# Optimization experiments

Measured on AMD Instinct MI355X. Metric: run time of the kernel, lower is better.

The kernel has to match this reference:

```python
import jax, jax.numpy as jnp
import numpy as np

D_MODEL = 1024
N_HEADS = 16
D_K = D_MODEL // N_HEADS
BATCH = 4
SEQ = 2048


def setup_inputs() -> dict:
    key = jax.random.key(0)
    ks = jax.random.split(key, 12)
    s = 1.0 / np.sqrt(D_MODEL)
    inp = {
        "query": jax.random.normal(ks[0], (BATCH, SEQ, D_MODEL), jnp.float32),
        "key": jax.random.normal(ks[1], (BATCH, SEQ, D_MODEL), jnp.float32),
        "value": jax.random.normal(ks[2], (BATCH, SEQ, D_MODEL), jnp.float32),
        # causal mask: True = masked (ignored), broadcastable over batch/heads
        "mask": jnp.triu(jnp.ones((SEQ, SEQ), bool), k=1)[None, None, :, :],
        "w_q": jax.random.normal(ks[3], (D_MODEL, D_MODEL), jnp.float32) * s,
        "b_q": jax.random.normal(ks[4], (D_MODEL,), jnp.float32) * s,
        "w_k": jax.random.normal(ks[5], (D_MODEL, D_MODEL), jnp.float32) * s,
        "b_k": jax.random.normal(ks[6], (D_MODEL,), jnp.float32) * s,
        "w_v": jax.random.normal(ks[7], (D_MODEL, D_MODEL), jnp.float32) * s,
        "b_v": jax.random.normal(ks[8], (D_MODEL,), jnp.float32) * s,
        "w_o": jax.random.normal(ks[9], (D_MODEL, D_MODEL), jnp.float32) * s,
        "b_o": jax.random.normal(ks[10], (D_MODEL,), jnp.float32) * s,
    }
    return inp


def _split_heads(x):
    # (B, S, D) -> (B, H, S, d_k)
    b, s, _ = x.shape
    return x.reshape(b, s, N_HEADS, D_K).transpose(0, 2, 1, 3)


def reference(query, key, value, mask, w_q, b_q, w_k, b_k, w_v, b_v, w_o, b_o):
    # torch Linear: y = x @ W.T + b
    q = _split_heads(query @ w_q.T + b_q)
    k = _split_heads(key @ w_k.T + b_k)
    v = _split_heads(value @ w_v.T + b_v)
    scale = 1.0 / jnp.sqrt(jnp.asarray(D_K, q.dtype))
    scores = jnp.einsum("bhqd,bhkd->bhqk", q, k) * scale
    scores = jnp.where(mask, jnp.asarray(-jnp.inf, scores.dtype), scores)
    weights = jax.nn.softmax(scores, axis=-1)  # dropout p=0.0 (eval)
    attn = jnp.einsum("bhqk,bhkd->bhqd", weights, v)
    b = attn.shape[0]
    attn = attn.transpose(0, 2, 1, 3).reshape(b, -1, D_MODEL)
    return attn @ w_o.T + b_o
```

## Files before the change

### kernel.cpp

```cpp
#include <hip/hip_runtime.h>

#define S_LEN 2048
#define DMODEL 1024
#define H_CNT 16
#define DK 64
#define BATCH 4

typedef __attribute__((ext_vector_type(8))) short short8;
typedef __attribute__((ext_vector_type(4))) float f32x4;
typedef __attribute__((ext_vector_type(16))) float f32x16;

static __device__ __forceinline__ short f2bf(float f) {
  union { float f; unsigned u; } x; x.f = f;
  unsigned r = x.u + 0x7fffu + ((x.u >> 16) & 1u);
  return (short)(r >> 16);
}

static __device__ __forceinline__ unsigned cvt_pk_bf16(float lo, float hi) {
  unsigned r;
  asm("v_cvt_pk_bf16_f32 %0, %1, %2" : "=v"(r) : "v"(lo), "v"(hi));
  return r;
}

static __device__ __forceinline__ void gl_lds16(const short* g, short* l) {
  __builtin_amdgcn_global_load_lds((const __attribute__((address_space(1))) void*)g,
                                   (__attribute__((address_space(3))) void*)l, 16, 0, 0);
}

__global__ __launch_bounds__(256) void cast_kernel(const float* __restrict__ src,
                                                   short* __restrict__ dst, int n8) {
  int i = blockIdx.x * 256 + threadIdx.x;
  if (i >= n8) return;
  const float4* s4 = (const float4*)src;
  float4 a = s4[2 * i], b = s4[2 * i + 1];
  short8 o;
  o[0] = f2bf(a.x); o[1] = f2bf(a.y); o[2] = f2bf(a.z); o[3] = f2bf(a.w);
  o[4] = f2bf(b.x); o[5] = f2bf(b.y); o[6] = f2bf(b.z); o[7] = f2bf(b.w);
  ((short8*)dst)[i] = o;
}

template <int MODE>
__global__ __launch_bounds__(256) void gemm_bt(const short* __restrict__ A,
                                               const short* __restrict__ B,
                                               const float* __restrict__ bias,
                                               void* __restrict__ Cout,
                                               int M, int N, int K, float scl) {
  __shared__ short Sab[(128 + 64) * 32];
  const int tid = threadIdx.x;
  const int lane = tid & 63, wid = tid >> 6;
  const int lin = blockIdx.x;
  const int w = (lin & 7) * 128 + (lin >> 3);
  int bx, by;
  if (MODE == 1) { bx = w >> 3; by = w & 7; }
  else           { bx = w & 15; by = w >> 4; }
  const int m0 = by * 128, n0 = bx * 64;
  const int wr = wid * 32;
  const int lrow = lane & 15, lk8 = (lane >> 4) * 8;

  const int l4 = lane >> 2, lc = (lane & 3) * 8;
  const short* gsrc[3];
  short* ldst[3];
#pragma unroll
  for (int i = 0; i < 3; i++) {
    int c = wid * 3 + i;
    ldst[i] = &Sab[c * 512];
    if (c < 8) gsrc[i] = &A[(size_t)(m0 + c * 16 + l4) * K + lc];
    else       gsrc[i] = &B[(size_t)(n0 + (c - 8) * 16 + l4) * K + lc];
  }

  f32x4 acc[2][4] = {};

  for (int k0 = 0; k0 < K; k0 += 32) {
#pragma unroll
    for (int i = 0; i < 3; i++) gl_lds16(gsrc[i] + k0, ldst[i]);
    __syncthreads();
    short8 af[2], bfr[4];
#pragma unroll
    for (int m = 0; m < 2; m++) af[m] = *(const short8*)(&Sab[(wr + m * 16 + lrow) * 32 + lk8]);
#pragma unroll
    for (int n = 0; n < 4; n++) bfr[n] = *(const short8*)(&Sab[(128 + n * 16 + lrow) * 32 + lk8]);
#pragma unroll
    for (int m = 0; m < 2; m++)
#pragma unroll
      for (int n = 0; n < 4; n++)
        acc[m][n] = __builtin_amdgcn_mfma_f32_16x16x32_bf16(af[m], bfr[n], acc[m][n], 0, 0, 0);
    __syncthreads();
  }

  const int g4 = (lane >> 4) * 4;
#pragma unroll
  for (int n = 0; n < 4; n++) {
    const int col = n0 + n * 16 + lrow;
#pragma unroll
    for (int m = 0; m < 2; m++) {
#pragma unroll
      for (int i = 0; i < 4; i++) {
        const int row = m0 + wr + m * 16 + g4 + i;
        float val = acc[m][n][i];
        if (MODE == 0) {
          val = (val + bias[col]) * scl;
          int b = row >> 11, s2 = row & 2047, h = col >> 6, d = col & 63;
          ((short*)Cout)[((size_t)(b * H_CNT + h) * S_LEN + s2) * DK + d] = f2bf(val);
        } else if (MODE == 1) {
          val = val + bias[row];
          int h = row >> 6, d = row & 63, b = col >> 11, s2 = col & 2047;
          ((short*)Cout)[((size_t)(b * H_CNT + h) * DK + d) * S_LEN + s2] = f2bf(val);
        } else {
          val = val + bias[col];
          ((float*)Cout)[(size_t)row * N + col] = val;
        }
      }
    }
  }
}

__global__ __launch_bounds__(256, 4) void attn2_kernel(const short* __restrict__ Q,
                                                       const short* __restrict__ Kc,
                                                       const short* __restrict__ Vt,
                                                       short* __restrict__ Oout) {
  const int bh = blockIdx.y;
  const int j = blockIdx.x;
  const int wid = threadIdx.x >> 6, lane = threadIdx.x & 63;
  const int qt = (wid == 0) ? j : (wid == 1) ? (31 - j) : (wid == 2) ? (32 + j) : (63 - j);
  const int q0 = qt * 32;
  const int ql = lane & 31, hl = lane >> 5;

  const short* Qb = Q + (size_t)bh * S_LEN * DK;
  const short* Kb = Kc + (size_t)bh * S_LEN * DK;
  const short* Vb = Vt + (size_t)bh * DK * S_LEN;

  short8 qf[4];
#pragma unroll
  for (int kk = 0; kk < 4; kk++)
    qf[kk] = *(const short8*)(&Qb[(q0 + ql) * DK + kk * 16 + hl * 8]);

  f32x16 oacc[2] = {};
  float mr = -1e30f, lr = 0.f;

  const int ntiles = qt + 1;
  for (int t = 0; t < ntiles; t++) {
    const int kv0 = t * 32;
    f32x16 st = {};
#pragma unroll
    for (int kk = 0; kk < 4; kk++) {
      short8 kf = *(const short8*)(&Kb[(kv0 + ql) * DK + kk * 16 + hl * 8]);
      st = __builtin_amdgcn_mfma_f32_32x32x16_bf16(kf, qf[kk], st, 0, 0, 0);
    }
    short8 vf[2][2];
#pragma unroll
    for (int td = 0; td < 2; td++)
#pragma unroll
      for (int kk = 0; kk < 2; kk++)
        vf[td][kk] = *(const short8*)(&Vb[(size_t)(td * 32 + ql) * S_LEN + kv0 + kk * 16 + hl * 8]);

    float p[16];
#pragma unroll
    for (int r = 0; r < 16; r++) p[r] = st[r];
    if (t == ntiles - 1) {
#pragma unroll
      for (int r = 0; r < 16; r++) {
        int kvr = (r & 3) + 8 * (r >> 2) + 4 * hl;
        if (kvr > ql) p[r] = -1e30f;
      }
    }
    float pm = p[0];
#pragma unroll
    for (int r = 1; r < 16; r++) pm = fmaxf(pm, p[r]);
    pm = fmaxf(pm, __shfl_xor(pm, 32, 64));
    if (!__all(pm <= mr + 8.f)) {
      float mnew = fmaxf(mr, pm);
      float al = __builtin_amdgcn_exp2f(mr - mnew);
      lr *= al;
#pragma unroll
      for (int td = 0; td < 2; td++)
#pragma unroll
        for (int r = 0; r < 16; r++) oacc[td][r] *= al;
      mr = mnew;
    }
    float rs = 0.f;
#pragma unroll
    for (int r = 0; r < 16; r++) {
      p[r] = __builtin_amdgcn_exp2f(p[r] - mr);
      rs += p[r];
    }
    rs += __shfl_xor(rs, 32, 64);
    lr += rs;

    unsigned wpk[8];
#pragma unroll
    for (int tt = 0; tt < 8; tt++) wpk[tt] = cvt_pk_bf16(p[2 * tt], p[2 * tt + 1]);
    union { short8 s; unsigned u[4]; } bf0, bf1;
    {
      unsigned xa = __shfl_xor((int)wpk[2], 32, 64), xb = __shfl_xor((int)wpk[0], 32, 64);
      bf0.u[0] = hl ? xa : wpk[0];
      bf0.u[2] = hl ? wpk[2] : xb;
    }
    {
      unsigned xa = __shfl_xor((int)wpk[3], 32, 64), xb = __shfl_xor((int)wpk[1], 32, 64);
      bf0.u[1] = hl ? xa : wpk[1];
      bf0.u[3] = hl ? wpk[3] : xb;
    }
    {
      unsigned xa = __shfl_xor((int)wpk[6], 32, 64), xb = __shfl_xor((int)wpk[4], 32, 64);
      bf1.u[0] = hl ? xa : wpk[4];
      bf1.u[2] = hl ? wpk[6] : xb;
    }
    {
      unsigned xa = __shfl_xor((int)wpk[7], 32, 64), xb = __shfl_xor((int)wpk[5], 32, 64);
      bf1.u[1] = hl ? xa : wpk[5];
      bf1.u[3] = hl ? wpk[7] : xb;
    }

#pragma unroll
    for (int td = 0; td < 2; td++) {
      oacc[td] = __builtin_amdgcn_mfma_f32_32x32x16_bf16(vf[td][0], bf0.s, oacc[td], 0, 0, 0);
      oacc[td] = __builtin_amdgcn_mfma_f32_32x32x16_bf16(vf[td][1], bf1.s, oacc[td], 0, 0, 0);
    }
  }

  const float inv = __builtin_amdgcn_rcpf(lr);
  const int b = bh >> 4, h = bh & 15;
  unsigned* ob = (unsigned*)Oout + ((size_t)b * S_LEN + q0 + ql) * (DMODEL / 2) + h * (DK / 2);
#pragma unroll
  for (int td = 0; td < 2; td++)
#pragma unroll
    for (int tt = 0; tt < 8; tt++) {
      unsigned pkv = cvt_pk_bf16(oacc[td][2 * tt] * inv, oacc[td][2 * tt + 1] * inv);
      ob[td * 16 + (tt & 1) + 4 * (tt >> 1) + 2 * hl] = pkv;
    }
}

extern "C" void kernel_launch(void* const* d_in, const int* in_sizes, int n_in,
                              void* d_out, int out_size, void* d_ws, size_t ws_size,
                              hipStream_t stream) {
  (void)in_sizes; (void)n_in; (void)out_size; (void)ws_size;
  const float* query = (const float*)d_in[0];
  const float* key_i = (const float*)d_in[1];
  const float* value = (const float*)d_in[2];
  const float* w_q = (const float*)d_in[4];
  const float* b_q = (const float*)d_in[5];
  const float* w_k = (const float*)d_in[6];
  const float* b_k = (const float*)d_in[7];
  const float* w_v = (const float*)d_in[8];
  const float* b_v = (const float*)d_in[9];
  const float* w_o = (const float*)d_in[10];
  const float* b_o = (const float*)d_in[11];

  const size_t XE = (size_t)BATCH * S_LEN * DMODEL;
  const size_t WE = (size_t)DMODEL * DMODEL;

  short* xq = (short*)d_ws;
  short* xk = xq + XE;
  short* xv = xk + XE;
  short* wq = xv + XE;
  short* wk = wq + WE;
  short* wv = wk + WE;
  short* wo = wv + WE;
  short* qb = wo + WE;
  short* kb = qb + XE;
  short* vtb = kb + XE;
  short* attnb = xq;

  const int M = BATCH * S_LEN;

  int n8x = (int)(XE / 8), n8w = (int)(WE / 8);
  cast_kernel<<<dim3((n8x + 255) / 256), 256, 0, stream>>>(query, xq, n8x);
  cast_kernel<<<dim3((n8x + 255) / 256), 256, 0, stream>>>(key_i, xk, n8x);
  cast_kernel<<<dim3((n8x + 255) / 256), 256, 0, stream>>>(value, xv, n8x);
  cast_kernel<<<dim3((n8w + 255) / 256), 256, 0, stream>>>(w_q, wq, n8w);
  cast_kernel<<<dim3((n8w + 255) / 256), 256, 0, stream>>>(w_k, wk, n8w);
  cast_kernel<<<dim3((n8w + 255) / 256), 256, 0, stream>>>(w_v, wv, n8w);
  cast_kernel<<<dim3((n8w + 255) / 256), 256, 0, stream>>>(w_o, wo, n8w);

  const float qscale = 0.125f * 1.44269504088896f;

  gemm_bt<0><<<1024, 256, 0, stream>>>(xq, wq, b_q, qb, M, DMODEL, DMODEL, qscale);
  gemm_bt<0><<<1024, 256, 0, stream>>>(xk, wk, b_k, kb, M, DMODEL, DMODEL, 1.f);
  gemm_bt<1><<<1024, 256, 0, stream>>>(wv, xv, b_v, vtb, DMODEL, M, DMODEL, 1.f);

  attn2_kernel<<<dim3(16, BATCH * H_CNT), 256, 0, stream>>>(qb, kb, vtb, attnb);

  gemm_bt<2><<<1024, 256, 0, stream>>>(attnb, wo, b_o, d_out, M, DMODEL, DMODEL, 1.f);
}
```

Measured before the change: 278.0 us.

## Enlarge GEMM tiles to 128x128 with K=64 and simplify softmax rescale

```diff
diff --git a/kernel.cpp b/kernel.cpp
--- a/kernel.cpp
+++ b/kernel.cpp
@@ -9,6 +9,7 @@
 typedef __attribute__((ext_vector_type(8))) short short8;
 typedef __attribute__((ext_vector_type(4))) float f32x4;
 typedef __attribute__((ext_vector_type(16))) float f32x16;
+typedef __attribute__((ext_vector_type(4))) unsigned uint4v;
 
 static __device__ __forceinline__ short f2bf(float f) {
   union { float f; unsigned u; } x; x.f = f;
@@ -16,10 +17,8 @@
   return (short)(r >> 16);
 }
 
-static __device__ __forceinline__ unsigned cvt_pk_bf16(float lo, float hi) {
-  unsigned r;
-  asm("v_cvt_pk_bf16_f32 %0, %1, %2" : "=v"(r) : "v"(lo), "v"(hi));
-  return r;
+static __device__ __forceinline__ unsigned pack_bf2(float lo, float hi) {
+  return (((unsigned)(unsigned short)f2bf(hi)) << 16) | ((unsigned)(unsigned short)f2bf(lo));
 }
 
 static __device__ __forceinline__ void gl_lds16(const short* g, short* l) {
@@ -40,59 +39,64 @@
 }
 
 template <int MODE>
-__global__ __launch_bounds__(256) void gemm_bt(const short* __restrict__ A,
-                                               const short* __restrict__ B,
-                                               const float* __restrict__ bias,
-                                               void* __restrict__ Cout,
-                                               int M, int N, int K, float scl) {
-  __shared__ short Sab[(128 + 64) * 32];
+__global__ __launch_bounds__(256) void gemm3(const short* __restrict__ A,
+                                             const short* __restrict__ B,
+                                             const float* __restrict__ bias,
+                                             void* __restrict__ Cout,
+                                             int M, int N, int K, float scl) {
+  __shared__ short As[128 * 64];
+  __shared__ short Bs[128 * 64];
   const int tid = threadIdx.x;
   const int lane = tid & 63, wid = tid >> 6;
   const int lin = blockIdx.x;
-  const int w = (lin & 7) * 128 + (lin >> 3);
+  const int w = (lin & 7) * 64 + (lin >> 3);
   int bx, by;
   if (MODE == 1) { bx = w >> 3; by = w & 7; }
-  else           { bx = w & 15; by = w >> 4; }
-  const int m0 = by * 128, n0 = bx * 64;
-  const int wr = wid * 32;
+  else           { bx = w & 7;  by = w >> 3; }
+  const int m0 = by * 128, n0 = bx * 128;
+  const int wr = (wid >> 1) * 64, wc = (wid & 1) * 64;
   const int lrow = lane & 15, lk8 = (lane >> 4) * 8;
 
-  const int l4 = lane >> 2, lc = (lane & 3) * 8;
-  const short* gsrc[3];
-  short* ldst[3];
-#pragma unroll
-  for (int i = 0; i < 3; i++) {
-    int c = wid * 3 + i;
-    ldst[i] = &Sab[c * 512];
-    if (c < 8) gsrc[i] = &A[(size_t)(m0 + c * 16 + l4) * K + lc];
-    else       gsrc[i] = &B[(size_t)(n0 + (c - 8) * 16 + l4) * K + lc];
-  }
-
-  f32x4 acc[2][4] = {};
-
-  for (int k0 = 0; k0 < K; k0 += 32) {
-#pragma unroll
-    for (int i = 0; i < 3; i++) gl_lds16(gsrc[i] + k0, ldst[i]);
+  const int srow = lane >> 3, scol = (lane & 7) * 8;
+  const int arow = m0 + wid * 32 + srow;
+  const int brow = n0 + wid * 32 + srow;
+
+  f32x4 acc[4][4] = {};
+
+  for (int k0 = 0; k0 < K; k0 += 64) {
+#pragma unroll
+    for (int i = 0; i < 4; i++) {
+      gl_lds16(&A[(size_t)(arow + i * 8) * K + k0 + scol], &As[(wid * 32 + i * 8) * 64]);
+      gl_lds16(&B[(size_t)(brow + i * 8) * K + k0 + scol], &Bs[(wid * 32 + i * 8) * 64]);
+    }
     __syncthreads();
-    short8 af[2], bfr[4];
-#pragma unroll
-    for (int m = 0; m < 2; m++) af[m] = *(const short8*)(&Sab[(wr + m * 16 + lrow) * 32 + lk8]);
-#pragma unroll
-    for (int n = 0; n < 4; n++) bfr[n] = *(const short8*)(&Sab[(128 + n * 16 + lrow) * 32 + lk8]);
-#pragma unroll
-    for (int m = 0; m < 2; m++)
-#pragma unroll
-      for (int n = 0; n < 4; n++)
-        acc[m][n] = __builtin_amdgcn_mfma_f32_16x16x32_bf16(af[m], bfr[n], acc[m][n], 0, 0, 0);
+    short8 af[4][2], bfr[4][2];
+#pragma unroll
+    for (int m = 0; m < 4; m++)
+#pragma unroll
+      for (int kk = 0; kk < 2; kk++)
+        af[m][kk] = *(const short8*)(&As[(wr + m * 16 + lrow) * 64 + kk * 32 + lk8]);
+#pragma unroll
+    for (int n = 0; n < 4; n++)
+#pragma unroll
+      for (int kk = 0; kk < 2; kk++)
+        bfr[n][kk] = *(const short8*)(&Bs[(wc + n * 16 + lrow) * 64 + kk * 32 + lk8]);
+#pragma unroll
+    for (int kk = 0; kk < 2; kk++)
+#pragma unroll
+      for (int m = 0; m < 4; m++)
+#pragma unroll
+        for (int n = 0; n < 4; n++)
+          acc[m][n] = __builtin_amdgcn_mfma_f32_16x16x32_bf16(af[m][kk], bfr[n][kk], acc[m][n], 0, 0, 0);
     __syncthreads();
   }
 
   const int g4 = (lane >> 4) * 4;
 #pragma unroll
   for (int n = 0; n < 4; n++) {
-    const int col = n0 + n * 16 + lrow;
-#pragma unroll
-    for (int m = 0; m < 2; m++) {
+    const int col = n0 + wc + n * 16 + lrow;
+#pragma unroll
+    for (int m = 0; m < 4; m++) {
 #pragma unroll
       for (int i = 0; i < 4; i++) {
         const int row = m0 + wr + m * 16 + g4 + i;
@@ -167,20 +171,19 @@
 #pragma unroll
     for (int r = 1; r < 16; r++) pm = fmaxf(pm, p[r]);
     pm = fmaxf(pm, __shfl_xor(pm, 32, 64));
-    if (!__all(pm <= mr + 8.f)) {
-      float mnew = fmaxf(mr, pm);
-      float al = __builtin_amdgcn_exp2f(mr - mnew);
-      lr *= al;
-#pragma unroll
-      for (int td = 0; td < 2; td++)
-#pragma unroll
-        for (int r = 0; r < 16; r++) oacc[td][r] *= al;
-      mr = mnew;
-    }
+    const float mnew = fmaxf(mr, pm);
+    const float al = __builtin_amdgcn_exp2f(mr - mnew);
+    mr = mnew;
+    lr *= al;
+#pragma unroll
+    for (int td = 0; td < 2; td++)
+#pragma unroll
+      for (int r = 0; r < 16; r++) oacc[td][r] *= al;
+
     float rs = 0.f;
 #pragma unroll
     for (int r = 0; r < 16; r++) {
-      p[r] = __builtin_amdgcn_exp2f(p[r] - mr);
+      p[r] = __builtin_amdgcn_exp2f(fminf(p[r] - mr, 0.f));
       rs += p[r];
     }
     rs += __shfl_xor(rs, 32, 64);
@@ -188,33 +191,35 @@
 
     unsigned wpk[8];
 #pragma unroll
-    for (int tt = 0; tt < 8; tt++) wpk[tt] = cvt_pk_bf16(p[2 * tt], p[2 * tt + 1]);
-    union { short8 s; unsigned u[4]; } bf0, bf1;
+    for (int tt = 0; tt < 8; tt++) wpk[tt] = pack_bf2(p[2 * tt], p[2 * tt + 1]);
+    uint4v u0, u1;
     {
       unsigned xa = __shfl_xor((int)wpk[2], 32, 64), xb = __shfl_xor((int)wpk[0], 32, 64);
-      bf0.u[0] = hl ? xa : wpk[0];
-      bf0.u[2] = hl ? wpk[2] : xb;
+      u0[0] = hl ? xa : wpk[0];
+      u0[2] = hl ? wpk[2] : xb;
     }
     {
       unsigned xa = __shfl_xor((int)wpk[3], 32, 64), xb = __shfl_xor((int)wpk[1], 32, 64);
-      bf0.u[1] = hl ? xa : wpk[1];
-      bf0.u[3] = hl ? wpk[3] : xb;
+      u0[1] = hl ? xa : wpk[1];
+      u0[3] = hl ? wpk[3] : xb;
     }
     {
       unsigned xa = __shfl_xor((int)wpk[6], 32, 64), xb = __shfl_xor((int)wpk[4], 32, 64);
-      bf1.u[0] = hl ? xa : wpk[4];
-      bf1.u[2] = hl ? wpk[6] : xb;
+      u1[0] = hl ? xa : wpk[4];
+      u1[2] = hl ? wpk[6] : xb;
     }
     {
       unsigned xa = __shfl_xor((int)wpk[7], 32, 64), xb = __shfl_xor((int)wpk[5], 32, 64);
-      bf1.u[1] = hl ? xa : wpk[5];
-      bf1.u[3] = hl ? wpk[7] : xb;
-    }
+      u1[1] = hl ? xa : wpk[5];
+      u1[3] = hl ? wpk[7] : xb;
+    }
+    const short8 pb0 = __builtin_bit_cast(short8, u0);
+    const short8 pb1 = __builtin_bit_cast(short8, u1);
 
 #pragma unroll
     for (int td = 0; td < 2; td++) {
-      oacc[td] = __builtin_amdgcn_mfma_f32_32x32x16_bf16(vf[td][0], bf0.s, oacc[td], 0, 0, 0);
-      oacc[td] = __builtin_amdgcn_mfma_f32_32x32x16_bf16(vf[td][1], bf1.s, oacc[td], 0, 0, 0);
+      oacc[td] = __builtin_amdgcn_mfma_f32_32x32x16_bf16(vf[td][0], pb0, oacc[td], 0, 0, 0);
+      oacc[td] = __builtin_amdgcn_mfma_f32_32x32x16_bf16(vf[td][1], pb1, oacc[td], 0, 0, 0);
     }
   }
 
@@ -225,7 +230,7 @@
   for (int td = 0; td < 2; td++)
 #pragma unroll
     for (int tt = 0; tt < 8; tt++) {
-      unsigned pkv = cvt_pk_bf16(oacc[td][2 * tt] * inv, oacc[td][2 * tt + 1] * inv);
+      unsigned pkv = pack_bf2(oacc[td][2 * tt] * inv, oacc[td][2 * tt + 1] * inv);
       ob[td * 16 + (tt & 1) + 4 * (tt >> 1) + 2 * hl] = pkv;
     }
 }
@@ -274,11 +279,11 @@
 
   const float qscale = 0.125f * 1.44269504088896f;
 
-  gemm_bt<0><<<1024, 256, 0, stream>>>(xq, wq, b_q, qb, M, DMODEL, DMODEL, qscale);
-  gemm_bt<0><<<1024, 256, 0, stream>>>(xk, wk, b_k, kb, M, DMODEL, DMODEL, 1.f);
-  gemm_bt<1><<<1024, 256, 0, stream>>>(wv, xv, b_v, vtb, DMODEL, M, DMODEL, 1.f);
+  gemm3<0><<<512, 256, 0, stream>>>(xq, wq, b_q, qb, M, DMODEL, DMODEL, qscale);
+  gemm3<0><<<512, 256, 0, stream>>>(xk, wk, b_k, kb, M, DMODEL, DMODEL, 1.f);
+  gemm3<1><<<512, 256, 0, stream>>>(wv, xv, b_v, vtb, DMODEL, M, DMODEL, 1.f);
 
   attn2_kernel<<<dim3(16, BATCH * H_CNT), 256, 0, stream>>>(qb, kb, vtb, attnb);
 
-  gemm_bt<2><<<1024, 256, 0, stream>>>(attnb, wo, b_o, d_out, M, DMODEL, DMODEL, 1.f);
-}
+  gemm3<2><<<512, 256, 0, stream>>>(attnb, wo, b_o, d_out, M, DMODEL, DMODEL, 1.f);
+}
```

Measured after the change: 286.3 us. +3.0%, slower.
